# Performance work log

Hardware: AMD Instinct MI355X
Metric: run time of the kernel (lower is better)

## Reference

```python
import jax, jax.numpy as jnp
import numpy as np

CL = 32      # config.cl (latent width)
NOBJ = 32    # config.num_obj
N = 1024     # batch


def _linear_params(key, fan_in, fan_out):
    w = jax.random.normal(key, (fan_in, fan_out), dtype=jnp.float32) / np.sqrt(fan_in)
    b = jnp.full((fan_out,), 0.1, dtype=jnp.float32)
    return w, b


def setup_inputs() -> dict:
    key = jax.random.key(0)
    keys = jax.random.split(key, 16)
    inp = {"s": jax.random.normal(keys[0], (N, NOBJ, CL // 2), dtype=jnp.float32)}
    specs = [
        ("state_enc", [(CL // 2, CL)]),
        ("self", [(CL, CL), (CL, CL)]),
        ("rel", [(2 * CL + 1, 2 * CL), (2 * CL, CL), (CL, CL)]),
        ("att", [(2 * CL + 1, 2 * CL), (2 * CL, CL), (CL, 1)]),
        ("aff", [(CL, CL), (CL, CL), (CL, CL)]),
        ("out", [(2 * CL, CL), (CL, CL)]),
    ]
    k = 1
    for name, shapes in specs:
        for j, (fi, fo) in enumerate(shapes):
            w, b = _linear_params(keys[k], fi, fo)
            k += 1
            if len(shapes) == 1:
                inp[name + "_w"], inp[name + "_b"] = w, b
            else:
                inp[name + "_w" + str(j)], inp[name + "_b" + str(j)] = w, b
    inp["core_idx"] = 0
    return inp


def _forward(s, state_enc_w, state_enc_b,
             self_w0, self_b0, self_w1, self_b1,
             rel_w0, rel_b0, rel_w1, rel_b1, rel_w2, rel_b2,
             att_w0, att_b0, att_w1, att_b1, att_w2, att_b2,
             aff_w0, aff_b0, aff_w1, aff_b1, aff_w2, aff_b2,
             out_w0, out_b0, out_w1, out_b1):
    # state encoding; keep raw (x, y) positions in the first 2 channels
    enc = s @ state_enc_w + state_enc_b                      # (n, o, cl)
    s2 = jnp.concatenate([s[..., :2], enc[..., 2:]], axis=-1)  # (n, o, cl)

    # self dynamics (residual MLP)
    h1 = jax.nn.relu(s2 @ self_w0 + self_b0)
    self_dyn = h1 @ self_w1 + self_b1 + h1                   # (n, o, cl)

    # pairwise squared distance over first two channels
    pos = s2[..., :2]
    diff = pos[:, :, None, :] - pos[:, None, :, :]           # (n, o, o, 2)
    dist = jnp.sum(diff * diff, axis=-1)                     # (n, o, o)

    # first layer of the edge MLPs applied to cat(obj_i, obj_j, dist) without
    # materializing the (n, o, o, 2cl+1) concat: split weight into W_i|W_j|w_d
    def pair_first(W, b):
        a = s2 @ W[:CL]                                      # (n, o, H)
        c = s2 @ W[CL:2 * CL]                                # (n, o, H)
        return a[:, :, None, :] + c[:, None, :, :] + dist[..., None] * W[2 * CL] + b

    # relation core (residual on last layer)
    rel1 = jax.nn.relu(pair_first(rel_w0, rel_b0))           # (n, o, o, 2cl)
    rel2 = jax.nn.relu(rel1 @ rel_w1 + rel_b1)               # (n, o, o, cl)
    rel_f = rel2 @ rel_w2 + rel_b2 + rel2                    # (n, o, o, cl)

    # attention net -> exp (unnormalized attention)
    att = jax.nn.relu(pair_first(att_w0, att_b0))
    att = jax.nn.relu(att @ att_w1 + att_b1)
    att = jnp.exp(att @ att_w2 + att_b2)                     # (n, o, o, 1)

    diag_mask = (1.0 - jnp.eye(NOBJ, dtype=s2.dtype))[None, :, :, None]
    rel_dyn = jnp.sum(rel_f * diag_mask * att, axis=2)       # (n, o, cl)

    dyn = self_dyn + rel_dyn

    # affector (tanh residual MLP)
    aff1 = jnp.tanh(dyn @ aff_w0 + aff_b0)
    aff2 = jnp.tanh(aff1 @ aff_w1 + aff_b1) + aff1
    aff3 = aff2 @ aff_w2 + aff_b2

    # output head
    aff_s = jnp.concatenate([aff3, s2], axis=-1)             # (n, o, 2cl)
    o1 = jnp.tanh(aff_s @ out_w0 + out_b0)
    result = o1 @ out_w1 + out_b1 + o1                       # (n, o, cl)
    return result


def reference(s, state_enc_w, state_enc_b,
              self_w0, self_b0, self_w1, self_b1,
              rel_w0, rel_b0, rel_w1, rel_b1, rel_w2, rel_b2,
              att_w0, att_b0, att_w1, att_b1, att_w2, att_b2,
              aff_w0, aff_b0, aff_w1, aff_b1, aff_w2, aff_b2,
              out_w0, out_b0, out_w1, out_b1, core_idx):
    # core_idx selects one of 3 identical cores in the original; only core 0
    # is materialized here (forward uses a single core).
    del core_idx
    return _forward(s, state_enc_w, state_enc_b,
                    self_w0, self_b0, self_w1, self_b1,
                    rel_w0, rel_b0, rel_w1, rel_b1, rel_w2, rel_b2,
                    att_w0, att_b0, att_w1, att_b1, att_w2, att_b2,
                    aff_w0, aff_b0, aff_w1, aff_b1, aff_w2, aff_b2,
                    out_w0, out_b0, out_w1, out_b1)
```

## Files before the change

kernel.cpp:

```cpp
#include <hip/hip_runtime.h>
#include <stdint.h>


enum : int {
  ENC_W  = 0,     ENC_B  = 512,
  SELF_W0 = 544,  SELF_B0 = 1568, SELF_W1 = 1600, SELF_B1 = 2624,
  REL_W0 = 2656,  REL_B0 = 6816,  REL_W1 = 6880,  REL_B1 = 8928,
  REL_W2 = 8960,  REL_B2 = 9984,
  ATT_W0 = 10016, ATT_B0 = 14176, ATT_W1 = 14240, ATT_B1 = 16288,
  ATT_W2 = 16320, ATT_B2 = 16352,
  AFF_W0 = 16356, AFF_B0 = 17380, AFF_W1 = 17412, AFF_B1 = 18436,
  AFF_W2 = 18468, AFF_B2 = 19492,
  OUT_W0 = 19524, OUT_B0 = 21572, OUT_W1 = 21604, OUT_B1 = 22628,
  W_FLAG = 22660,
  W_TOTAL = 22661
};

__device__ __forceinline__ float bf2f(uint16_t h) {
  union { uint32_t u; float f; } v; v.u = ((uint32_t)h) << 16; return v.f;
}
__device__ __forceinline__ uint16_t f2bf(float f) {
  union { float f; uint32_t u; } v; v.f = f;
  uint32_t r = (v.u + 0x7fffu + ((v.u >> 16) & 1u)) >> 16;
  return (uint16_t)r;
}

struct ConvArgs {
  const void* src[28];
  const uint32_t* probe;
  int size[28];
  int off[28];
};

__global__ void dyn_conv_kernel(ConvArgs a, float* __restrict__ W) {
  const int t = blockIdx.x;
  const bool is_fp32 = (*a.probe == 0x3DCCCCCDu);
  const int cnt = a.size[t];
  float* d = W + a.off[t];
  if (is_fp32) {
    const float* s = (const float*)a.src[t];
    for (int e = threadIdx.x; e < cnt; e += blockDim.x) d[e] = s[e];
  } else {
    const uint16_t* s = (const uint16_t*)a.src[t];
    for (int e = threadIdx.x; e < cnt; e += blockDim.x) d[e] = bf2f(s[e]);
  }
  if (t == 0 && threadIdx.x == 0) W[W_FLAG] = is_fp32 ? 1.f : 0.f;
}

struct ArenaPair {
  float pa[32][68];
  float pc[32][68];
};
struct ArenaPost {
  float rd[32][36];
  float t1[32][36];
  float t2[32][36];
};
struct ArenaEarly {
  float s[32][16];
  float h1[32][33];
};
union ArenaU {
  ArenaPair a;
  ArenaPost b;
  ArenaEarly c;
};

__global__ __launch_bounds__(256, 2) void dyn_main_kernel(
    const void* __restrict__ Sv,
    const float* __restrict__ Wf,
    void* __restrict__ OUTv)
{
  __shared__ __align__(16) ArenaU u;
  __shared__ float sh_s2[32][33];
  __shared__ float sh_dist[32][33];
  __shared__ float sh_sd[32][33];
  __shared__ float sh_wdr[64];
  __shared__ float sh_wda[64];
  __shared__ __align__(16) float sh_wtA[2048];
  __shared__ __align__(16) float sh_wtB[2048];
  __shared__ float sh_misc[100];

  const int tid = threadIdx.x;
  const int n   = blockIdx.x;
  const int i8  = tid >> 3;
  const int l8  = tid & 7;
  const int m0  = l8 << 2;

  const bool is_fp32 = (Wf[W_FLAG] != 0.f);

  const float4* wtA4 = (const float4*)sh_wtA;
  const float4* wtB4 = (const float4*)sh_wtB;

  auto stage = [&](float* dst, int off, int n4) {
    const float4* src = (const float4*)(Wf + off);
    float4* d4 = (float4*)dst;
    for (int q = tid; q < n4; q += 256) d4[q] = src[q];
  };

  {
    const int e = tid * 2;
    if (is_fp32) {
      const float* sp = (const float*)Sv + (size_t)n * 512;
      u.c.s[e >> 4][e & 15]             = sp[e];
      u.c.s[(e + 1) >> 4][(e + 1) & 15] = sp[e + 1];
    } else {
      const uint16_t* sp = (const uint16_t*)Sv + (size_t)n * 512;
      u.c.s[e >> 4][e & 15]             = bf2f(sp[e]);
      u.c.s[(e + 1) >> 4][(e + 1) & 15] = bf2f(sp[e + 1]);
    }
    stage(sh_wtA, ENC_W, 128);
  }
  __syncthreads();

  {
    float e0 = Wf[ENC_B + m0 + 0], e1 = Wf[ENC_B + m0 + 1];
    float e2 = Wf[ENC_B + m0 + 2], e3 = Wf[ENC_B + m0 + 3];
    #pragma unroll
    for (int c = 0; c < 16; ++c) {
      const float sc = u.c.s[i8][c];
      const float4 w = wtA4[c * 8 + l8];
      e0 = fmaf(sc, w.x, e0); e1 = fmaf(sc, w.y, e1);
      e2 = fmaf(sc, w.z, e2); e3 = fmaf(sc, w.w, e3);
    }
    if (m0 == 0) { e0 = u.c.s[i8][0]; e1 = u.c.s[i8][1]; }
    sh_s2[i8][m0 + 0] = e0; sh_s2[i8][m0 + 1] = e1;
    sh_s2[i8][m0 + 2] = e2; sh_s2[i8][m0 + 3] = e3;
    stage(sh_wtB, SELF_W0, 256);
  }
  __syncthreads();

  {
    const float xi = sh_s2[i8][0], yi = sh_s2[i8][1];
    #pragma unroll
    for (int q = 0; q < 4; ++q) {
      const int j = m0 + q;
      const float dx = xi - sh_s2[j][0];
      const float dy = yi - sh_s2[j][1];
      sh_dist[i8][j] = dx * dx + dy * dy;
    }
  }
  {
    float a0 = Wf[SELF_B0 + m0 + 0], a1 = Wf[SELF_B0 + m0 + 1];
    float a2 = Wf[SELF_B0 + m0 + 2], a3 = Wf[SELF_B0 + m0 + 3];
    #pragma unroll
    for (int k = 0; k < 32; ++k) {
      const float x = sh_s2[i8][k];
      const float4 w = wtB4[k * 8 + l8];
      a0 = fmaf(x, w.x, a0); a1 = fmaf(x, w.y, a1);
      a2 = fmaf(x, w.z, a2); a3 = fmaf(x, w.w, a3);
    }
    u.c.h1[i8][m0 + 0] = fmaxf(a0, 0.f); u.c.h1[i8][m0 + 1] = fmaxf(a1, 0.f);
    u.c.h1[i8][m0 + 2] = fmaxf(a2, 0.f); u.c.h1[i8][m0 + 3] = fmaxf(a3, 0.f);
    stage(sh_wtA, SELF_W1, 256);
  }
  __syncthreads();

  {
    float a0 = Wf[SELF_B1 + m0 + 0], a1 = Wf[SELF_B1 + m0 + 1];
    float a2 = Wf[SELF_B1 + m0 + 2], a3 = Wf[SELF_B1 + m0 + 3];
    #pragma unroll
    for (int k = 0; k < 32; ++k) {
      const float x = u.c.h1[i8][k];
      const float4 w = wtA4[k * 8 + l8];
      a0 = fmaf(x, w.x, a0); a1 = fmaf(x, w.y, a1);
      a2 = fmaf(x, w.z, a2); a3 = fmaf(x, w.w, a3);
    }
    sh_sd[i8][m0 + 0] = a0 + u.c.h1[i8][m0 + 0];
    sh_sd[i8][m0 + 1] = a1 + u.c.h1[i8][m0 + 1];
    sh_sd[i8][m0 + 2] = a2 + u.c.h1[i8][m0 + 2];
    sh_sd[i8][m0 + 3] = a3 + u.c.h1[i8][m0 + 3];
  }
  __syncthreads();

  auto precompute_ac = [&](int W0base, int B0base) {
    const int arr = tid >> 7;
    const int row = (tid >> 2) & 31;
    const int k0  = (tid & 3) * 16;
    const float* bb = Wf + B0base + k0;
    const float bs = (arr == 0) ? 1.f : 0.f;
    float acc[16];
    #pragma unroll
    for (int kk = 0; kk < 16; ++kk) acc[kk] = bs * bb[kk];
    const float* wb = Wf + W0base + arr * 2048 + k0;
    for (int c = 0; c < 32; ++c) {
      const float sc = sh_s2[row][c];
      const float* w = wb + c * 64;
      #pragma unroll
      for (int kk = 0; kk < 16; kk += 4) {
        const float4 wv = *(const float4*)&w[kk];
        acc[kk + 0] = fmaf(sc, wv.x, acc[kk + 0]);
        acc[kk + 1] = fmaf(sc, wv.y, acc[kk + 1]);
        acc[kk + 2] = fmaf(sc, wv.z, acc[kk + 2]);
        acc[kk + 3] = fmaf(sc, wv.w, acc[kk + 3]);
      }
    }
    float* dst = (arr == 0) ? &u.a.pa[row][k0] : &u.a.pc[row][k0];
    #pragma unroll
    for (int kk = 0; kk < 16; kk += 4)
      *(float4*)&dst[kk] = make_float4(acc[kk], acc[kk+1], acc[kk+2], acc[kk+3]);
  };

  if (tid < 64)        sh_wdr[tid]      = Wf[REL_W0 + 64 * 64 + tid];
  else if (tid < 128)  sh_wda[tid - 64] = Wf[ATT_W0 + 64 * 64 + (tid - 64)];
  stage(sh_wtB, ATT_W1, 512);
  if (tid < 97)
    sh_misc[tid] = Wf[tid < 32 ? REL_B1 + tid
                    : tid < 64 ? ATT_B1 + (tid - 32)
                    : tid < 96 ? ATT_W2 + (tid - 64) : ATT_B2];
  precompute_ac(ATT_W0, ATT_B0);
  __syncthreads();

  stage(sh_wtA, REL_W1, 512);
  auto att_pair = [&](int p) -> float {
    asm volatile("" ::: "memory");
    const int j = l8 + 8 * p;
    const float d = sh_dist[i8][j];
    const float4* A = (const float4*)&u.a.pa[i8][0];
    const float4* C = (const float4*)&u.a.pc[j][0];
    const float4* D = (const float4*)&sh_wda[0];
    float v[32];
    #pragma unroll
    for (int m = 0; m < 32; ++m) v[m] = sh_misc[32 + m];
    #pragma unroll 1
    for (int kq = 0; kq < 16; ++kq) {
      const float4 av = A[kq], cv = C[kq], wv = D[kq];
      const float x0 = fmaxf(fmaf(d, wv.x, av.x + cv.x), 0.f);
      const float x1 = fmaxf(fmaf(d, wv.y, av.y + cv.y), 0.f);
      const float x2 = fmaxf(fmaf(d, wv.z, av.z + cv.z), 0.f);
      const float x3 = fmaxf(fmaf(d, wv.w, av.w + cv.w), 0.f);
      const float4* wb = wtB4 + kq * 32;
      #pragma unroll
      for (int mq = 0; mq < 8; ++mq) {
        const float4 w0 = wb[mq], w1 = wb[8+mq], w2 = wb[16+mq], w3 = wb[24+mq];
        float t;
        t = fmaf(x0, w0.x, v[mq*4+0]); t = fmaf(x1, w1.x, t);
        t = fmaf(x2, w2.x, t);         v[mq*4+0] = fmaf(x3, w3.x, t);
        t = fmaf(x0, w0.y, v[mq*4+1]); t = fmaf(x1, w1.y, t);
        t = fmaf(x2, w2.y, t);         v[mq*4+1] = fmaf(x3, w3.y, t);
        t = fmaf(x0, w0.z, v[mq*4+2]); t = fmaf(x1, w1.z, t);
        t = fmaf(x2, w2.z, t);         v[mq*4+2] = fmaf(x3, w3.z, t);
        t = fmaf(x0, w0.w, v[mq*4+3]); t = fmaf(x1, w1.w, t);
        t = fmaf(x2, w2.w, t);         v[mq*4+3] = fmaf(x3, w3.w, t);
      }
    }
    float s0 = sh_misc[96], s1 = 0.f, s2 = 0.f, s3 = 0.f;
    #pragma unroll
    for (int k = 0; k < 32; k += 4) {
      s0 = fmaf(fmaxf(v[k + 0], 0.f), sh_misc[64 + k + 0], s0);
      s1 = fmaf(fmaxf(v[k + 1], 0.f), sh_misc[64 + k + 1], s1);
      s2 = fmaf(fmaxf(v[k + 2], 0.f), sh_misc[64 + k + 2], s2);
      s3 = fmaf(fmaxf(v[k + 3], 0.f), sh_misc[64 + k + 3], s3);
    }
    const float lg = (s0 + s1) + (s2 + s3);
    return (j == i8) ? 0.f : expf(lg);
  };
  const float e0 = att_pair(0);
  const float e1 = att_pair(1);
  const float e2 = att_pair(2);
  const float e3 = att_pair(3);
  float E = (e0 + e1) + (e2 + e3);
  __syncthreads();

  precompute_ac(REL_W0, REL_B0);
  stage(sh_wtB, REL_W2, 256);
  __syncthreads();

  float g[32];
  #pragma unroll
  for (int m = 0; m < 32; ++m) g[m] = 0.f;

  auto rel_pair = [&](int p, float e) {
    asm volatile("" ::: "memory");
    const int j = l8 + 8 * p;
    const float d = sh_dist[i8][j];
    const float4* A = (const float4*)&u.a.pa[i8][0];
    const float4* C = (const float4*)&u.a.pc[j][0];
    const float4* D = (const float4*)&sh_wdr[0];
    float v[32];
    #pragma unroll
    for (int m = 0; m < 32; ++m) v[m] = sh_misc[m];
    #pragma unroll 1
    for (int kq = 0; kq < 16; ++kq) {
      const float4 av = A[kq], cv = C[kq], wv = D[kq];
      const float x0 = fmaxf(fmaf(d, wv.x, av.x + cv.x), 0.f);
      const float x1 = fmaxf(fmaf(d, wv.y, av.y + cv.y), 0.f);
      const float x2 = fmaxf(fmaf(d, wv.z, av.z + cv.z), 0.f);
      const float x3 = fmaxf(fmaf(d, wv.w, av.w + cv.w), 0.f);
      const float4* wb = wtA4 + kq * 32;
      #pragma unroll
      for (int mq = 0; mq < 8; ++mq) {
        const float4 w0 = wb[mq], w1 = wb[8+mq], w2 = wb[16+mq], w3 = wb[24+mq];
        float t;
        t = fmaf(x0, w0.x, v[mq*4+0]); t = fmaf(x1, w1.x, t);
        t = fmaf(x2, w2.x, t);         v[mq*4+0] = fmaf(x3, w3.x, t);
        t = fmaf(x0, w0.y, v[mq*4+1]); t = fmaf(x1, w1.y, t);
        t = fmaf(x2, w2.y, t);         v[mq*4+1] = fmaf(x3, w3.y, t);
        t = fmaf(x0, w0.z, v[mq*4+2]); t = fmaf(x1, w1.z, t);
        t = fmaf(x2, w2.z, t);         v[mq*4+2] = fmaf(x3, w3.z, t);
        t = fmaf(x0, w0.w, v[mq*4+3]); t = fmaf(x1, w1.w, t);
        t = fmaf(x2, w2.w, t);         v[mq*4+3] = fmaf(x3, w3.w, t);
      }
    }
    #pragma unroll
    for (int m = 0; m < 32; ++m)
      g[m] = fmaf(e, fmaxf(v[m], 0.f), g[m]);
  };
  rel_pair(0, e0);
  rel_pair(1, e1);
  rel_pair(2, e2);
  rel_pair(3, e3);

  #pragma unroll
  for (int m = 0; m < 32; ++m) {
    float vv = g[m];
    vv += __shfl_xor(vv, 1);
    vv += __shfl_xor(vv, 2);
    vv += __shfl_xor(vv, 4);
    g[m] = vv;
  }
  E += __shfl_xor(E, 1);
  E += __shfl_xor(E, 2);
  E += __shfl_xor(E, 4);
  __syncthreads();
  if (l8 == 0) {
    #pragma unroll
    for (int q = 0; q < 8; ++q)
      *(float4*)&u.b.t1[i8][q * 4] =
          make_float4(g[q * 4], g[q * 4 + 1], g[q * 4 + 2], g[q * 4 + 3]);
    u.b.t1[i8][32] = E;
  }
  __syncthreads();

  {
    stage(sh_wtA, AFF_W0, 256);
    const float Ei = u.b.t1[i8][32];
    float a0 = fmaf(Ei, Wf[REL_B2 + m0 + 0], u.b.t1[i8][m0 + 0]);
    float a1 = fmaf(Ei, Wf[REL_B2 + m0 + 1], u.b.t1[i8][m0 + 1]);
    float a2 = fmaf(Ei, Wf[REL_B2 + m0 + 2], u.b.t1[i8][m0 + 2]);
    float a3 = fmaf(Ei, Wf[REL_B2 + m0 + 3], u.b.t1[i8][m0 + 3]);
    #pragma unroll
    for (int k = 0; k < 32; ++k) {
      const float x = u.b.t1[i8][k];
      const float4 w = wtB4[k * 8 + l8];
      a0 = fmaf(x, w.x, a0); a1 = fmaf(x, w.y, a1);
      a2 = fmaf(x, w.z, a2); a3 = fmaf(x, w.w, a3);
    }
    __syncthreads();
    u.b.rd[i8][m0 + 0] = a0; u.b.rd[i8][m0 + 1] = a1;
    u.b.rd[i8][m0 + 2] = a2; u.b.rd[i8][m0 + 3] = a3;
  }
  __syncthreads();

  {
    stage(sh_wtB, AFF_W1, 256);
    float a0 = Wf[AFF_B0 + m0 + 0], a1 = Wf[AFF_B0 + m0 + 1];
    float a2 = Wf[AFF_B0 + m0 + 2], a3 = Wf[AFF_B0 + m0 + 3];
    #pragma unroll
    for (int k = 0; k < 32; ++k) {
      const float x = sh_sd[i8][k] + u.b.rd[i8][k];
      const float4 w = wtA4[k * 8 + l8];
      a0 = fmaf(x, w.x, a0); a1 = fmaf(x, w.y, a1);
      a2 = fmaf(x, w.z, a2); a3 = fmaf(x, w.w, a3);
    }
    u.b.t1[i8][m0 + 0] = tanhf(a0); u.b.t1[i8][m0 + 1] = tanhf(a1);
    u.b.t1[i8][m0 + 2] = tanhf(a2); u.b.t1[i8][m0 + 3] = tanhf(a3);
  }
  __syncthreads();

  {
    stage(sh_wtA, AFF_W2, 256);
    float a0 = Wf[AFF_B1 + m0 + 0], a1 = Wf[AFF_B1 + m0 + 1];
    float a2 = Wf[AFF_B1 + m0 + 2], a3 = Wf[AFF_B1 + m0 + 3];
    #pragma unroll
    for (int k = 0; k < 32; ++k) {
      const float x = u.b.t1[i8][k];
      const float4 w = wtB4[k * 8 + l8];
      a0 = fmaf(x, w.x, a0); a1 = fmaf(x, w.y, a1);
      a2 = fmaf(x, w.z, a2); a3 = fmaf(x, w.w, a3);
    }
    u.b.t2[i8][m0 + 0] = tanhf(a0) + u.b.t1[i8][m0 + 0];
    u.b.t2[i8][m0 + 1] = tanhf(a1) + u.b.t1[i8][m0 + 1];
    u.b.t2[i8][m0 + 2] = tanhf(a2) + u.b.t1[i8][m0 + 2];
    u.b.t2[i8][m0 + 3] = tanhf(a3) + u.b.t1[i8][m0 + 3];
  }
  __syncthreads();

  {
    stage(sh_wtB, OUT_W0, 512);
    float a0 = Wf[AFF_B2 + m0 + 0], a1 = Wf[AFF_B2 + m0 + 1];
    float a2 = Wf[AFF_B2 + m0 + 2], a3 = Wf[AFF_B2 + m0 + 3];
    #pragma unroll
    for (int k = 0; k < 32; ++k) {
      const float x = u.b.t2[i8][k];
      const float4 w = wtA4[k * 8 + l8];
      a0 = fmaf(x, w.x, a0); a1 = fmaf(x, w.y, a1);
      a2 = fmaf(x, w.z, a2); a3 = fmaf(x, w.w, a3);
    }
    u.b.t1[i8][m0 + 0] = a0; u.b.t1[i8][m0 + 1] = a1;
    u.b.t1[i8][m0 + 2] = a2; u.b.t1[i8][m0 + 3] = a3;
  }
  __syncthreads();

  {
    stage(sh_wtA, OUT_W1, 256);
    float a0 = Wf[OUT_B0 + m0 + 0], a1 = Wf[OUT_B0 + m0 + 1];
    float a2 = Wf[OUT_B0 + m0 + 2], a3 = Wf[OUT_B0 + m0 + 3];
    #pragma unroll
    for (int k = 0; k < 32; ++k) {
      const float x1 = u.b.t1[i8][k];
      const float4 wa = wtB4[k * 8 + l8];
      a0 = fmaf(x1, wa.x, a0); a1 = fmaf(x1, wa.y, a1);
      a2 = fmaf(x1, wa.z, a2); a3 = fmaf(x1, wa.w, a3);
      const float x2 = sh_s2[i8][k];
      const float4 wbv = wtB4[256 + k * 8 + l8];
      a0 = fmaf(x2, wbv.x, a0); a1 = fmaf(x2, wbv.y, a1);
      a2 = fmaf(x2, wbv.z, a2); a3 = fmaf(x2, wbv.w, a3);
    }
    u.b.t2[i8][m0 + 0] = tanhf(a0); u.b.t2[i8][m0 + 1] = tanhf(a1);
    u.b.t2[i8][m0 + 2] = tanhf(a2); u.b.t2[i8][m0 + 3] = tanhf(a3);
  }
  __syncthreads();

  {
    float a0 = Wf[OUT_B1 + m0 + 0], a1 = Wf[OUT_B1 + m0 + 1];
    float a2 = Wf[OUT_B1 + m0 + 2], a3 = Wf[OUT_B1 + m0 + 3];
    #pragma unroll
    for (int k = 0; k < 32; ++k) {
      const float x = u.b.t2[i8][k];
      const float4 w = wtA4[k * 8 + l8];
      a0 = fmaf(x, w.x, a0); a1 = fmaf(x, w.y, a1);
      a2 = fmaf(x, w.z, a2); a3 = fmaf(x, w.w, a3);
    }
    a0 += u.b.t2[i8][m0 + 0]; a1 += u.b.t2[i8][m0 + 1];
    a2 += u.b.t2[i8][m0 + 2]; a3 += u.b.t2[i8][m0 + 3];
    const size_t idx = (size_t)n * 1024 + i8 * 32 + m0;
    if (is_fp32) {
      *(float4*)&((float*)OUTv)[idx] = make_float4(a0, a1, a2, a3);
    } else {
      ushort4 r;
      r.x = f2bf(a0); r.y = f2bf(a1); r.z = f2bf(a2); r.w = f2bf(a3);
      *(ushort4*)&((uint16_t*)OUTv)[idx] = r;
    }
  }
}

extern "C" void kernel_launch(void* const* d_in, const int* in_sizes, int n_in,
                              void* d_out, int out_size, void* d_ws, size_t ws_size,
                              hipStream_t stream) {
  (void)in_sizes; (void)n_in; (void)out_size; (void)ws_size;
  static const int sizes[28] = {
    512, 32, 1024, 32, 1024, 32,
    4160, 64, 2048, 32, 1024, 32,
    4160, 64, 2048, 32, 32, 1,
    1024, 32, 1024, 32, 1024, 32,
    2048, 32, 1024, 32};
  static const int offs[28] = {
    ENC_W, ENC_B, SELF_W0, SELF_B0, SELF_W1, SELF_B1,
    REL_W0, REL_B0, REL_W1, REL_B1, REL_W2, REL_B2,
    ATT_W0, ATT_B0, ATT_W1, ATT_B1, ATT_W2, ATT_B2,
    AFF_W0, AFF_B0, AFF_W1, AFF_B1, AFF_W2, AFF_B2,
    OUT_W0, OUT_B0, OUT_W1, OUT_B1};

  ConvArgs ca;
  for (int i = 0; i < 28; ++i) {
    ca.src[i]  = d_in[1 + i];
    ca.size[i] = sizes[i];
    ca.off[i]  = offs[i];
  }
  ca.probe = (const uint32_t*)d_in[2];
  float* W = (float*)d_ws;
  hipLaunchKernelGGL(dyn_conv_kernel, dim3(28), dim3(256), 0, stream, ca, W);
  hipLaunchKernelGGL(dyn_main_kernel, dim3(1024), dim3(256), 0, stream,
                     d_in[0], (const float*)W, d_out);
}
```

Baseline: 363.5 us.

## Split pair MLP output channels across lane halves, two pairs per thread

Changes the work split in the attention and relation pair MLPs. Each thread now computes half of the 32 hidden outputs for two j-pairs at once, instead of all 32 outputs for one pair. Each weight float4 loaded from LDS is reused across two pairs, which halves the weight LDS reads per FMA, and the per-thread accumulator arrays shrink from 32 to 16. The cost is an extra cross-lane shuffle to combine attention logits, a changed reduction pattern, and two writer lanes for the output row.

```diff
diff --git a/kernel.cpp b/kernel.cpp
--- a/kernel.cpp
+++ b/kernel.cpp
@@ -86,6 +86,9 @@
   const int i8  = tid >> 3;
   const int l8  = tid & 7;
   const int m0  = l8 << 2;
+  const int jg  = l8 & 3;
+  const int h16 = (l8 >> 2) << 4;
+  const int h4  = (l8 >> 2) << 2;
 
   const bool is_fp32 = (Wf[W_FLAG] != 0.f);
 
@@ -212,123 +215,167 @@
   __syncthreads();
 
   stage(sh_wtA, REL_W1, 512);
-  auto att_pair = [&](int p) -> float {
+  auto att_pair2 = [&](int p) -> float2 {
     asm volatile("" ::: "memory");
-    const int j = l8 + 8 * p;
-    const float d = sh_dist[i8][j];
-    const float4* A = (const float4*)&u.a.pa[i8][0];
-    const float4* C = (const float4*)&u.a.pc[j][0];
-    const float4* D = (const float4*)&sh_wda[0];
-    float v[32];
-    #pragma unroll
-    for (int m = 0; m < 32; ++m) v[m] = sh_misc[32 + m];
+    const int j1 = jg + 8 * p;
+    const int j2 = jg + 4 + 8 * p;
+    const float d1 = sh_dist[i8][j1];
+    const float d2 = sh_dist[i8][j2];
+    const float4* A  = (const float4*)&u.a.pa[i8][0];
+    const float4* C1 = (const float4*)&u.a.pc[j1][0];
+    const float4* C2 = (const float4*)&u.a.pc[j2][0];
+    const float4* D  = (const float4*)&sh_wda[0];
+    float v1[16], v2[16];
+    #pragma unroll
+    for (int m = 0; m < 16; ++m) { v1[m] = sh_misc[32 + h16 + m]; v2[m] = v1[m]; }
     #pragma unroll 1
     for (int kq = 0; kq < 16; ++kq) {
-      const float4 av = A[kq], cv = C[kq], wv = D[kq];
-      const float x0 = fmaxf(fmaf(d, wv.x, av.x + cv.x), 0.f);
-      const float x1 = fmaxf(fmaf(d, wv.y, av.y + cv.y), 0.f);
-      const float x2 = fmaxf(fmaf(d, wv.z, av.z + cv.z), 0.f);
-      const float x3 = fmaxf(fmaf(d, wv.w, av.w + cv.w), 0.f);
-      const float4* wb = wtB4 + kq * 32;
+      const float4 av = A[kq], c1 = C1[kq], c2 = C2[kq], wv = D[kq];
+      const float x0 = fmaxf(fmaf(d1, wv.x, av.x + c1.x), 0.f);
+      const float x1 = fmaxf(fmaf(d1, wv.y, av.y + c1.y), 0.f);
+      const float x2 = fmaxf(fmaf(d1, wv.z, av.z + c1.z), 0.f);
+      const float x3 = fmaxf(fmaf(d1, wv.w, av.w + c1.w), 0.f);
+      const float y0 = fmaxf(fmaf(d2, wv.x, av.x + c2.x), 0.f);
+      const float y1 = fmaxf(fmaf(d2, wv.y, av.y + c2.y), 0.f);
+      const float y2 = fmaxf(fmaf(d2, wv.z, av.z + c2.z), 0.f);
+      const float y3 = fmaxf(fmaf(d2, wv.w, av.w + c2.w), 0.f);
+      const float4* wb = wtB4 + kq * 32 + h4;
       #pragma unroll
-      for (int mq = 0; mq < 8; ++mq) {
+      for (int mq = 0; mq < 4; ++mq) {
         const float4 w0 = wb[mq], w1 = wb[8+mq], w2 = wb[16+mq], w3 = wb[24+mq];
         float t;
-        t = fmaf(x0, w0.x, v[mq*4+0]); t = fmaf(x1, w1.x, t);
-        t = fmaf(x2, w2.x, t);         v[mq*4+0] = fmaf(x3, w3.x, t);
-        t = fmaf(x0, w0.y, v[mq*4+1]); t = fmaf(x1, w1.y, t);
-        t = fmaf(x2, w2.y, t);         v[mq*4+1] = fmaf(x3, w3.y, t);
-        t = fmaf(x0, w0.z, v[mq*4+2]); t = fmaf(x1, w1.z, t);
-        t = fmaf(x2, w2.z, t);         v[mq*4+2] = fmaf(x3, w3.z, t);
-        t = fmaf(x0, w0.w, v[mq*4+3]); t = fmaf(x1, w1.w, t);
-        t = fmaf(x2, w2.w, t);         v[mq*4+3] = fmaf(x3, w3.w, t);
+        t = fmaf(x0, w0.x, v1[mq*4+0]); t = fmaf(x1, w1.x, t);
+        t = fmaf(x2, w2.x, t);          v1[mq*4+0] = fmaf(x3, w3.x, t);
+        t = fmaf(y0, w0.x, v2[mq*4+0]); t = fmaf(y1, w1.x, t);
+        t = fmaf(y2, w2.x, t);          v2[mq*4+0] = fmaf(y3, w3.x, t);
+        t = fmaf(x0, w0.y, v1[mq*4+1]); t = fmaf(x1, w1.y, t);
+        t = fmaf(x2, w2.y, t);          v1[mq*4+1] = fmaf(x3, w3.y, t);
+        t = fmaf(y0, w0.y, v2[mq*4+1]); t = fmaf(y1, w1.y, t);
+        t = fmaf(y2, w2.y, t);          v2[mq*4+1] = fmaf(y3, w3.y, t);
+        t = fmaf(x0, w0.z, v1[mq*4+2]); t = fmaf(x1, w1.z, t);
+        t = fmaf(x2, w2.z, t);          v1[mq*4+2] = fmaf(x3, w3.z, t);
+        t = fmaf(y0, w0.z, v2[mq*4+2]); t = fmaf(y1, w1.z, t);
+        t = fmaf(y2, w2.z, t);          v2[mq*4+2] = fmaf(y3, w3.z, t);
+        t = fmaf(x0, w0.w, v1[mq*4+3]); t = fmaf(x1, w1.w, t);
+        t = fmaf(x2, w2.w, t);          v1[mq*4+3] = fmaf(x3, w3.w, t);
+        t = fmaf(y0, w0.w, v2[mq*4+3]); t = fmaf(y1, w1.w, t);
+        t = fmaf(y2, w2.w, t);          v2[mq*4+3] = fmaf(y3, w3.w, t);
       }
     }
-    float s0 = sh_misc[96], s1 = 0.f, s2 = 0.f, s3 = 0.f;
-    #pragma unroll
-    for (int k = 0; k < 32; k += 4) {
-      s0 = fmaf(fmaxf(v[k + 0], 0.f), sh_misc[64 + k + 0], s0);
-      s1 = fmaf(fmaxf(v[k + 1], 0.f), sh_misc[64 + k + 1], s1);
-      s2 = fmaf(fmaxf(v[k + 2], 0.f), sh_misc[64 + k + 2], s2);
-      s3 = fmaf(fmaxf(v[k + 3], 0.f), sh_misc[64 + k + 3], s3);
-    }
-    const float lg = (s0 + s1) + (s2 + s3);
-    return (j == i8) ? 0.f : expf(lg);
+    float la0 = 0.f, la1 = 0.f, lb0 = 0.f, lb1 = 0.f;
+    #pragma unroll
+    for (int k = 0; k < 16; k += 2) {
+      la0 = fmaf(fmaxf(v1[k + 0], 0.f), sh_misc[64 + h16 + k + 0], la0);
+      la1 = fmaf(fmaxf(v1[k + 1], 0.f), sh_misc[64 + h16 + k + 1], la1);
+      lb0 = fmaf(fmaxf(v2[k + 0], 0.f), sh_misc[64 + h16 + k + 0], lb0);
+      lb1 = fmaf(fmaxf(v2[k + 1], 0.f), sh_misc[64 + h16 + k + 1], lb1);
+    }
+    float lg1 = la0 + la1;
+    float lg2 = lb0 + lb1;
+    lg1 += __shfl_xor(lg1, 4);
+    lg2 += __shfl_xor(lg2, 4);
+    lg1 += sh_misc[96];
+    lg2 += sh_misc[96];
+    float2 r;
+    r.x = (j1 == i8) ? 0.f : expf(lg1);
+    r.y = (j2 == i8) ? 0.f : expf(lg2);
+    return r;
   };
-  const float e0 = att_pair(0);
-  const float e1 = att_pair(1);
-  const float e2 = att_pair(2);
-  const float e3 = att_pair(3);
-  float E = (e0 + e1) + (e2 + e3);
+  const float2 ep0 = att_pair2(0);
+  const float2 ep1 = att_pair2(1);
+  const float2 ep2 = att_pair2(2);
+  const float2 ep3 = att_pair2(3);
+  float E = ((ep0.x + ep0.y) + (ep1.x + ep1.y))
+          + ((ep2.x + ep2.y) + (ep3.x + ep3.y));
   __syncthreads();
 
   precompute_ac(REL_W0, REL_B0);
   stage(sh_wtB, REL_W2, 256);
   __syncthreads();
 
-  float g[32];
+  float g[16];
   #pragma unroll
-  for (int m = 0; m < 32; ++m) g[m] = 0.f;
-
-  auto rel_pair = [&](int p, float e) {
+  for (int m = 0; m < 16; ++m) g[m] = 0.f;
+
+  auto rel_pair2 = [&](int p, float e1, float e2) {
     asm volatile("" ::: "memory");
-    const int j = l8 + 8 * p;
-    const float d = sh_dist[i8][j];
-    const float4* A = (const float4*)&u.a.pa[i8][0];
-    const float4* C = (const float4*)&u.a.pc[j][0];
-    const float4* D = (const float4*)&sh_wdr[0];
-    float v[32];
-    #pragma unroll
-    for (int m = 0; m < 32; ++m) v[m] = sh_misc[m];
+    const int j1 = jg + 8 * p;
+    const int j2 = jg + 4 + 8 * p;
+    const float d1 = sh_dist[i8][j1];
+    const float d2 = sh_dist[i8][j2];
+    const float4* A  = (const float4*)&u.a.pa[i8][0];
+    const float4* C1 = (const float4*)&u.a.pc[j1][0];
+    const float4* C2 = (const float4*)&u.a.pc[j2][0];
+    const float4* D  = (const float4*)&sh_wdr[0];
+    float v1[16], v2[16];
+    #pragma unroll
+    for (int m = 0; m < 16; ++m) { v1[m] = sh_misc[h16 + m]; v2[m] = v1[m]; }
     #pragma unroll 1
     for (int kq = 0; kq < 16; ++kq) {
-      const float4 av = A[kq], cv = C[kq], wv = D[kq];
-      const float x0 = fmaxf(fmaf(d, wv.x, av.x + cv.x), 0.f);
-      const float x1 = fmaxf(fmaf(d, wv.y, av.y + cv.y), 0.f);
-      const float x2 = fmaxf(fmaf(d, wv.z, av.z + cv.z), 0.f);
-      const float x3 = fmaxf(fmaf(d, wv.w, av.w + cv.w), 0.f);
-      const float4* wb = wtA4 + kq * 32;
+      const float4 av = A[kq], c1 = C1[kq], c2 = C2[kq], wv = D[kq];
+      const float x0 = fmaxf(fmaf(d1, wv.x, av.x + c1.x), 0.f);
+      const float x1 = fmaxf(fmaf(d1, wv.y, av.y + c1.y), 0.f);
+      const float x2 = fmaxf(fmaf(d1, wv.z, av.z + c1.z), 0.f);
+      const float x3 = fmaxf(fmaf(d1, wv.w, av.w + c1.w), 0.f);
+      const float y0 = fmaxf(fmaf(d2, wv.x, av.x + c2.x), 0.f);
+      const float y1 = fmaxf(fmaf(d2, wv.y, av.y + c2.y), 0.f);
+      const float y2 = fmaxf(fmaf(d2, wv.z, av.z + c2.z), 0.f);
+      const float y3 = fmaxf(fmaf(d2, wv.w, av.w + c2.w), 0.f);
+      const float4* wb = wtA4 + kq * 32 + h4;
       #pragma unroll
-      for (int mq = 0; mq < 8; ++mq) {
+      for (int mq = 0; mq < 4; ++mq) {
         const float4 w0 = wb[mq], w1 = wb[8+mq], w2 = wb[16+mq], w3 = wb[24+mq];
         float t;
-        t = fmaf(x0, w0.x, v[mq*4+0]); t = fmaf(x1, w1.x, t);
-        t = fmaf(x2, w2.x, t);         v[mq*4+0] = fmaf(x3, w3.x, t);
-        t = fmaf(x0, w0.y, v[mq*4+1]); t = fmaf(x1, w1.y, t);
-        t = fmaf(x2, w2.y, t);         v[mq*4+1] = fmaf(x3, w3.y, t);
-        t = fmaf(x0, w0.z, v[mq*4+2]); t = fmaf(x1, w1.z, t);
-        t = fmaf(x2, w2.z, t);         v[mq*4+2] = fmaf(x3, w3.z, t);
-        t = fmaf(x0, w0.w, v[mq*4+3]); t = fmaf(x1, w1.w, t);
-        t = fmaf(x2, w2.w, t);         v[mq*4+3] = fmaf(x3, w3.w, t);
+        t = fmaf(x0, w0.x, v1[mq*4+0]); t = fmaf(x1, w1.x, t);
+        t = fmaf(x2, w2.x, t);          v1[mq*4+0] = fmaf(x3, w3.x, t);
+        t = fmaf(y0, w0.x, v2[mq*4+0]); t = fmaf(y1, w1.x, t);
+        t = fmaf(y2, w2.x, t);          v2[mq*4+0] = fmaf(y3, w3.x, t);
+        t = fmaf(x0, w0.y, v1[mq*4+1]); t = fmaf(x1, w1.y, t);
+        t = fmaf(x2, w2.y, t);          v1[mq*4+1] = fmaf(x3, w3.y, t);
+        t = fmaf(y0, w0.y, v2[mq*4+1]); t = fmaf(y1, w1.y, t);
+        t = fmaf(y2, w2.y, t);          v2[mq*4+1] = fmaf(y3, w3.y, t);
+        t = fmaf(x0, w0.z, v1[mq*4+2]); t = fmaf(x1, w1.z, t);
+        t = fmaf(x2, w2.z, t);          v1[mq*4+2] = fmaf(x3, w3.z, t);
+        t = fmaf(y0, w0.z, v2[mq*4+2]); t = fmaf(y1, w1.z, t);
+        t = fmaf(y2, w2.z, t);          v2[mq*4+2] = fmaf(y3, w3.z, t);
+        t = fmaf(x0, w0.w, v1[mq*4+3]); t = fmaf(x1, w1.w, t);
+        t = fmaf(x2, w2.w, t);          v1[mq*4+3] = fmaf(x3, w3.w, t);
+        t = fmaf(y0, w0.w, v2[mq*4+3]); t = fmaf(y1, w1.w, t);
+        t = fmaf(y2, w2.w, t);          v2[mq*4+3] = fmaf(y3, w3.w, t);
       }
     }
     #pragma unroll
-    for (int m = 0; m < 32; ++m)
-      g[m] = fmaf(e, fmaxf(v[m], 0.f), g[m]);
+    for (int m = 0; m < 16; ++m) {
+      g[m] = fmaf(e1, fmaxf(v1[m], 0.f), g[m]);
+      g[m] = fmaf(e2, fmaxf(v2[m], 0.f), g[m]);
+    }
   };
-  rel_pair(0, e0);
-  rel_pair(1, e1);
-  rel_pair(2, e2);
-  rel_pair(3, e3);
+  rel_pair2(0, ep0.x, ep0.y);
+  rel_pair2(1, ep1.x, ep1.y);
+  rel_pair2(2, ep2.x, ep2.y);
+  rel_pair2(3, ep3.x, ep3.y);
 
   #pragma unroll
-  for (int m = 0; m < 32; ++m) {
+  for (int m = 0; m < 16; ++m) {
     float vv = g[m];
     vv += __shfl_xor(vv, 1);
     vv += __shfl_xor(vv, 2);
-    vv += __shfl_xor(vv, 4);
     g[m] = vv;
   }
   E += __shfl_xor(E, 1);
   E += __shfl_xor(E, 2);
-  E += __shfl_xor(E, 4);
   __syncthreads();
   if (l8 == 0) {
     #pragma unroll
-    for (int q = 0; q < 8; ++q)
+    for (int q = 0; q < 4; ++q)
       *(float4*)&u.b.t1[i8][q * 4] =
           make_float4(g[q * 4], g[q * 4 + 1], g[q * 4 + 2], g[q * 4 + 3]);
     u.b.t1[i8][32] = E;
+  } else if (l8 == 4) {
+    #pragma unroll
+    for (int q = 0; q < 4; ++q)
+      *(float4*)&u.b.t1[i8][16 + q * 4] =
+          make_float4(g[q * 4], g[q * 4 + 1], g[q * 4 + 2], g[q * 4 + 3]);
   }
   __syncthreads();
 
```

After: 324.1 us. 1.12x faster.
